# Optimization experiments

Measured on AMD Instinct MI355X. Metric: run time of the kernel, lower is better.

Reference implementation:

```python
import jax, jax.numpy as jnp
import numpy as np

D_MODEL = 128; D_STATE = 64; D_CONV = 4; EXPAND = 2; HEADDIM = 32; NGROUPS = 1
D_INNER = EXPAND * D_MODEL            # 256
NHEADS = D_INNER // HEADDIM           # 8
CONV_DIM = D_INNER + 2 * NGROUPS * D_STATE   # 384 (x, B, C streams)
D_IN_PROJ = 2 * D_INNER + 2 * NGROUPS * D_STATE + NHEADS  # 648 (z, xBC, dt)
EPS = 1e-5


def setup_inputs() -> dict:
    key = jax.random.key(0)
    ks = jax.random.split(key, 8)
    B, L = 8, 4096
    x = jax.random.normal(ks[0], (B, L, D_MODEL), jnp.float32)
    norm_w = jnp.ones((D_MODEL,), jnp.float32)
    in_proj_w = jax.random.normal(ks[1], (D_IN_PROJ, D_MODEL), jnp.float32) * (D_MODEL ** -0.5)
    conv_w = jax.random.normal(ks[2], (CONV_DIM, D_CONV), jnp.float32) * (D_CONV ** -0.5)
    conv_b = jnp.zeros((CONV_DIM,), jnp.float32)
    dt_bias = jax.random.uniform(ks[3], (NHEADS,), jnp.float32, -4.0, -1.0)
    A_log = jnp.log(jax.random.uniform(ks[4], (NHEADS,), jnp.float32, 1.0, 16.0))
    D = jnp.ones((NHEADS,), jnp.float32)
    gnorm_w = jnp.ones((D_INNER,), jnp.float32)
    out_proj_w = jax.random.normal(ks[5], (D_MODEL, D_INNER), jnp.float32) * (D_INNER ** -0.5)
    return dict(x=x, norm_w=norm_w, in_proj_w=in_proj_w, conv_w=conv_w, conv_b=conv_b,
                dt_bias=dt_bias, A_log=A_log, D=D, gnorm_w=gnorm_w, out_proj_w=out_proj_w)


def _rmsnorm(x, w):
    return x * jax.lax.rsqrt(jnp.mean(x * x, axis=-1, keepdims=True) + EPS) * w


def _causal_dw_conv(x, w, b):
    # x: [B,L,C]; w: [C,K]; depthwise causal conv along L
    K = w.shape[1]
    xp = jnp.pad(x, ((0, 0), (K - 1, 0), (0, 0)))
    kern = jnp.transpose(w)[:, None, :]  # [K,1,C] for WIO with groups=C
    out = jax.lax.conv_general_dilated(
        xp, kern, window_strides=(1,), padding='VALID',
        dimension_numbers=('NWC', 'WIO', 'NWC'),
        feature_group_count=w.shape[0])
    return out + b


def _ssm(xh, dt, Bm, Cm, A):
    # xh: [B,L,H,P]; dt: [B,L,H]; Bm, Cm: [B,L,N]; A: [H]
    def step(h, inp):
        x_t, dt_t, B_t, C_t = inp
        dA = jnp.exp(dt_t * A)                                   # [B,H]
        h = h * dA[..., None, None] + (dt_t[..., None] * x_t)[..., None] * B_t[:, None, None, :]
        y = jnp.einsum('bhpn,bn->bhp', h, C_t)
        return h, y
    Bsz, L, H, P = xh.shape
    N = Bm.shape[-1]
    h0 = jnp.zeros((Bsz, H, P, N), xh.dtype)
    xs = (xh.transpose(1, 0, 2, 3), dt.transpose(1, 0, 2),
          Bm.transpose(1, 0, 2), Cm.transpose(1, 0, 2))
    _, ys = jax.lax.scan(step, h0, xs)
    return ys.transpose(1, 0, 2, 3)  # [B,L,H,P]


def reference(x, norm_w, in_proj_w, conv_w, conv_b, dt_bias, A_log, D, gnorm_w, out_proj_w):
    xn = _rmsnorm(x, norm_w)
    zxbcdt = xn @ in_proj_w.T                                    # [B,L,648]
    z, xBC, dt = jnp.split(zxbcdt, [D_INNER, D_INNER + CONV_DIM], axis=-1)
    dt = jax.nn.softplus(dt + dt_bias)                           # [B,L,H]
    xBC = jax.nn.silu(_causal_dw_conv(xBC, conv_w, conv_b))
    xs, Bm, Cm = jnp.split(xBC, [D_INNER, D_INNER + NGROUPS * D_STATE], axis=-1)
    Bsz, L, _ = x.shape
    xh = xs.reshape(Bsz, L, NHEADS, HEADDIM)
    A = -jnp.exp(A_log)                                          # [H]
    y = _ssm(xh, dt, Bm, Cm, A) + D[None, None, :, None] * xh    # D skip per head
    y = y.reshape(Bsz, L, D_INNER)
    y = _rmsnorm(y * jax.nn.silu(z), gnorm_w)                    # gated RMSNorm
    out = y @ out_proj_w.T
    return x + out
```

## Files before the change

### kernel.cpp

```cpp
#include <hip/hip_runtime.h>

#define DM    128
#define DI    256
#define NH    8
#define HD    32
#define NS    64
#define CDIM  384
#define DPROJ 648
#define LSEQ  4096
#define NB    8
#define NTOK  32768
#define LC    64
#define NC    64
#define EPSF  1e-5f
#define LOG2E 1.4426950408889634f

typedef __bf16 bf16;
typedef bf16  bf16x8 __attribute__((ext_vector_type(8)));
typedef bf16  bf16x4 __attribute__((ext_vector_type(4)));
typedef short short8 __attribute__((ext_vector_type(8)));
typedef float f32x4  __attribute__((ext_vector_type(4)));

__device__ __forceinline__ unsigned short f2bfbits(float f) {
    unsigned int u = __float_as_uint(f);
    unsigned int r = u + 0x7FFFu + ((u >> 16) & 1u);
    return (unsigned short)(r >> 16);
}
__device__ __forceinline__ float bfbits2f(unsigned short u) {
    return __uint_as_float(((unsigned int)u) << 16);
}

__global__ __launch_bounds__(256) void k_prep(const float* __restrict__ w1,
                                              const float* __restrict__ w2,
                                              const float* __restrict__ gw,
                                              unsigned short* __restrict__ w1g,
                                              unsigned short* __restrict__ w2f) {
    int i = blockIdx.x * 256 + threadIdx.x;
    if (i < 640 * DM) {
        int f = i >> 9, r = i & 511;
        int lane = r >> 3, jj = r & 7;
        int ns = f >> 2, kk = f & 3;
        int n = ns * 16 + (lane & 15), k = kk * 32 + (lane >> 4) * 8 + jj;
        w1g[i] = f2bfbits(w1[(size_t)n * DM + k]);
    } else {
        int j = i - 640 * DM;
        if (j < DM * DI) {
            int f = j >> 9, r = j & 511;
            int lane = r >> 3, jj = r & 7;
            int kk = f >> 3, nt = f & 7;
            int fr = lane & 15, ko = lane >> 4;
            int n = nt * 16 + fr, k = kk * 32 + ko * 8 + jj;
            w2f[j] = f2bfbits(w2[(size_t)n * DI + k] * gw[k]);
        }
    }
}

__global__ __launch_bounds__(256, 4) void k_gemm1(const float* __restrict__ x,
                                                  const float* __restrict__ nw,
                                                  const float* __restrict__ w1,
                                                  const float* __restrict__ dtb,
                                                  const unsigned short* __restrict__ w1g,
                                                  unsigned short* __restrict__ zb,
                                                  unsigned short* __restrict__ xbc,
                                                  float* __restrict__ dtf) {
    __shared__ float Xs[64][132];
    __shared__ float Wd[8][132];
    const int t = threadIdx.x;
    const int wave = t >> 6, lane = t & 63;
    const int m0 = blockIdx.x * 64;
    {
        int row = t >> 5, col = (t & 31) * 4;
        *(float4*)&Wd[row][col] = *(const float4*)(w1 + (size_t)(640 + row) * DM + col);
    }
    const float nw0 = nw[lane * 2], nw1 = nw[lane * 2 + 1];
    #pragma unroll
    for (int i = 0; i < 16; i++) {
        int r = wave * 16 + i;
        const float* xr = x + (size_t)(m0 + r) * DM + lane * 2;
        float v0 = xr[0], v1 = xr[1];
        float ss = v0 * v0 + v1 * v1;
        #pragma unroll
        for (int o = 32; o; o >>= 1) ss += __shfl_xor(ss, o);
        float rs = rsqrtf(ss * (1.0f / DM) + EPSF);
        Xs[r][lane * 2]     = v0 * rs * nw0;
        Xs[r][lane * 2 + 1] = v1 * rs * nw1;
    }
    __syncthreads();
    {
        const int h = lane >> 3, ks = lane & 7;
        const float dtbh = dtb[h];
        #pragma unroll
        for (int i = 0; i < 16; i++) {
            int r = wave * 16 + i;
            float acc = 0.f;
            #pragma unroll
            for (int q = 0; q < 4; q++) {
                float4 xv = *(const float4*)&Xs[r][ks * 16 + q * 4];
                float4 wv = *(const float4*)&Wd[h][ks * 16 + q * 4];
                acc = fmaf(xv.x, wv.x, acc); acc = fmaf(xv.y, wv.y, acc);
                acc = fmaf(xv.z, wv.z, acc); acc = fmaf(xv.w, wv.w, acc);
            }
            acc += __shfl_xor(acc, 1);
            acc += __shfl_xor(acc, 2);
            acc += __shfl_xor(acc, 4);
            if (ks == 0) {
                float v = acc + dtbh;
                dtf[(size_t)(m0 + r) * NH + h] = (v > 20.f) ? v : log1pf(expf(v));
            }
        }
    }
    const int wm = wave >> 1, wn = wave & 1;
    const int fr = lane & 15, ko = lane >> 4;
    bf16x8 a[2][4];
    #pragma unroll
    for (int mt = 0; mt < 2; mt++)
        #pragma unroll
        for (int kk = 0; kk < 4; kk++) {
            const float* src = &Xs[wm * 32 + mt * 16 + fr][kk * 32 + ko * 8];
            float4 lo = *(const float4*)src, hi = *(const float4*)(src + 4);
            bf16x8 af;
            af[0] = (bf16)lo.x; af[1] = (bf16)lo.y; af[2] = (bf16)lo.z; af[3] = (bf16)lo.w;
            af[4] = (bf16)hi.x; af[5] = (bf16)hi.y; af[6] = (bf16)hi.z; af[7] = (bf16)hi.w;
            a[mt][kk] = af;
        }
    for (int nt = 0; nt < 10; nt++) {
        const unsigned short* wb = w1g + (((size_t)(nt * 4 + wn * 2) * 4) << 9) + lane * 8;
        f32x4 acc[2][2] = {};
        #pragma unroll
        for (int kk = 0; kk < 4; kk++) {
            bf16x8 b0 = *(const bf16x8*)(wb + ((size_t)kk << 9));
            bf16x8 b1 = *(const bf16x8*)(wb + ((size_t)(4 + kk) << 9));
            acc[0][0] = __builtin_amdgcn_mfma_f32_16x16x32_bf16(a[0][kk], b0, acc[0][0], 0, 0, 0);
            acc[1][0] = __builtin_amdgcn_mfma_f32_16x16x32_bf16(a[1][kk], b0, acc[1][0], 0, 0, 0);
            acc[0][1] = __builtin_amdgcn_mfma_f32_16x16x32_bf16(a[0][kk], b1, acc[0][1], 0, 0, 0);
            acc[1][1] = __builtin_amdgcn_mfma_f32_16x16x32_bf16(a[1][kk], b1, acc[1][1], 0, 0, 0);
        }
        unsigned short* dst; int ld, nc0;
        if (nt < 4) { dst = zb;  ld = DI;   nc0 = nt * 64; }
        else        { dst = xbc; ld = CDIM; nc0 = nt * 64 - 256; }
        #pragma unroll
        for (int mt = 0; mt < 2; mt++)
            #pragma unroll
            for (int ntt = 0; ntt < 2; ntt++) {
                int n = nc0 + wn * 32 + ntt * 16 + fr;
                #pragma unroll
                for (int rr = 0; rr < 4; rr++) {
                    int m = m0 + wm * 32 + mt * 16 + ko * 4 + rr;
                    dst[(size_t)m * ld + n] = f2bfbits(acc[mt][ntt][rr]);
                }
            }
    }
}

__global__ __launch_bounds__(384) void k_conv(const unsigned short* __restrict__ xbc,
                                              const float* __restrict__ cw,
                                              const float* __restrict__ cb,
                                              unsigned short* __restrict__ bcA,
                                              unsigned short* __restrict__ xT,
                                              unsigned short* __restrict__ bT) {
    __shared__ __align__(16) unsigned short L[320][72];
    const int c = threadIdx.x;
    const int t0 = blockIdx.x * 64;
    const int l0 = t0 & (LSEQ - 1);
    float4 wv = *(const float4*)(cw + c * 4);
    float bias = cb[c];
    const unsigned short* in = xbc + (size_t)t0 * CDIM + c;
    float h1 = 0.f, h2 = 0.f, h3 = 0.f;
    if (l0) {
        h1 = bfbits2f(in[-CDIM]);
        h2 = bfbits2f(in[-2 * CDIM]);
        h3 = bfbits2f(in[-3 * CDIM]);
    }
    short8 pk;
    #pragma unroll 8
    for (int t = 0; t < 64; t++) {
        float x0 = bfbits2f(in[(size_t)t * CDIM]);
        float acc = bias;
        acc = fmaf(x0, wv.w, acc);
        acc = fmaf(h1, wv.z, acc);
        acc = fmaf(h2, wv.y, acc);
        acc = fmaf(h3, wv.x, acc);
        float s = acc / (1.f + expf(-acc));
        unsigned short us = f2bfbits(s);
        if (c >= 256) bcA[(size_t)(t0 + t) * 128 + (c - 256)] = us;
        pk[t & 7] = (short)us;
        if (c < 320 && (t & 7) == 7) *(short8*)&L[c][t - 7] = pk;
        h3 = h2; h2 = h1; h1 = x0;
    }
    __syncthreads();
    #pragma unroll
    for (int it = 0; it < 7; it++) {
        int idx = it * 384 + c;
        if (idx < 2560) {
            int row = idx >> 3, tc = (idx & 7) * 8;
            short8 v = *(const short8*)&L[row][tc];
            unsigned short* dst = (row < 256)
                ? xT + (size_t)row * NTOK + t0 + tc
                : bT + (size_t)(row - 256) * NTOK + t0 + tc;
            *(short8*)dst = v;
        }
    }
}

__global__ __launch_bounds__(256, 4) void k_ssd1(const unsigned short* __restrict__ bT,
                                                 const unsigned short* __restrict__ xT,
                                                 const float* __restrict__ dtf,
                                                 const float* __restrict__ alog,
                                                 unsigned short* __restrict__ hst,
                                                 float* __restrict__ dAp) {
    __shared__ __align__(16) float wl[4][64];
    const int bh = blockIdx.x >> 4, cg = blockIdx.x & 15;
    const int b = bh >> 3, h = bh & 7;
    const int wave = threadIdx.x >> 6, lane = threadIdx.x & 63;
    const int c = cg * 4 + wave;
    const size_t tok0 = (size_t)b * LSEQ + c * LC;
    const float A = -expf(alog[h]);
    float dt = dtf[(tok0 + lane) * NH + h];
    float q = dt * A * LOG2E;
    #pragma unroll
    for (int o = 1; o <= 32; o <<= 1) {
        float tmp = __shfl_up(q, o);
        if (lane >= o) q += tmp;
    }
    float qL = __shfl(q, 63);
    wl[wave][lane] = exp2f(qL - q) * dt;
    if (lane == 0) dAp[(size_t)bh * NC + c] = exp2f(qL);
    const int m = lane & 15, ko = lane >> 4;
    f32x4 hacc[4][2] = {};
    #pragma unroll
    for (int kh = 0; kh < 2; kh++) {
        bf16x8 xb[2];
        #pragma unroll
        for (int pi = 0; pi < 2; pi++)
            xb[pi] = *(const bf16x8*)(xT + (size_t)(h * HD + pi * 16 + m) * NTOK + tok0 + kh * 32 + ko * 8);
        f32x4 w0 = *(const f32x4*)&wl[wave][kh * 32 + ko * 8];
        f32x4 w1 = *(const f32x4*)&wl[wave][kh * 32 + ko * 8 + 4];
        #pragma unroll
        for (int ni = 0; ni < 4; ni++) {
            bf16x8 bv = *(const bf16x8*)(bT + (size_t)(ni * 16 + m) * NTOK + tok0 + kh * 32 + ko * 8);
            bf16x8 af;
            #pragma unroll
            for (int j = 0; j < 4; j++) af[j] = (bf16)((float)bv[j] * w0[j]);
            #pragma unroll
            for (int j = 0; j < 4; j++) af[4 + j] = (bf16)((float)bv[4 + j] * w1[j]);
            #pragma unroll
            for (int pi = 0; pi < 2; pi++)
                hacc[ni][pi] = __builtin_amdgcn_mfma_f32_16x16x32_bf16(af, xb[pi], hacc[ni][pi], 0, 0, 0);
        }
    }
    unsigned short* hb = hst + (((size_t)bh * NC + c) << 11);
    #pragma unroll
    for (int ni = 0; ni < 4; ni++)
        #pragma unroll
        for (int pi = 0; pi < 2; pi++) {
            bf16x4 pv;
            #pragma unroll
            for (int r = 0; r < 4; r++) pv[r] = (bf16)hacc[ni][pi][r];
            *(bf16x4*)(hb + (pi * 16 + m) * 64 + ni * 16 + ko * 4) = pv;
        }
}

__global__ __launch_bounds__(256) void k_ssm2(unsigned short* __restrict__ hst,
                                              const float* __restrict__ dAp) {
    __shared__ float dl[NC];
    const int bh = blockIdx.x >> 3, seg = blockIdx.x & 7;
    const int s = seg * 256 + threadIdx.x;
    if (threadIdx.x < NC) dl[threadIdx.x] = dAp[(size_t)bh * NC + threadIdx.x];
    __syncthreads();
    unsigned short* p = hst + ((size_t)bh * NC << 11) + s;
    float r = 0.f;
    float v0 = bfbits2f(p[0]);
    float v1 = bfbits2f(p[(size_t)1 << 11]);
    float v2 = bfbits2f(p[(size_t)2 << 11]);
    float v3 = bfbits2f(p[(size_t)3 << 11]);
    for (int c = 0; c < NC; c += 4) {
        float t;
        t = v0; if (c + 4 < NC) v0 = bfbits2f(p[(size_t)(c + 4) << 11]);
        p[(size_t)c << 11] = f2bfbits(r);       r = fmaf(r, dl[c], t);
        t = v1; if (c + 5 < NC) v1 = bfbits2f(p[(size_t)(c + 5) << 11]);
        p[(size_t)(c + 1) << 11] = f2bfbits(r); r = fmaf(r, dl[c + 1], t);
        t = v2; if (c + 6 < NC) v2 = bfbits2f(p[(size_t)(c + 6) << 11]);
        p[(size_t)(c + 2) << 11] = f2bfbits(r); r = fmaf(r, dl[c + 2], t);
        t = v3; if (c + 7 < NC) v3 = bfbits2f(p[(size_t)(c + 7) << 11]);
        p[(size_t)(c + 3) << 11] = f2bfbits(r); r = fmaf(r, dl[c + 3], t);
    }
}

__global__ __launch_bounds__(256, 2) void k_ssd3(const unsigned short* __restrict__ bcA,
                                                 const unsigned short* __restrict__ xT,
                                                 const float* __restrict__ dtf,
                                                 const float* __restrict__ alog,
                                                 const unsigned short* __restrict__ hst,
                                                 const float* __restrict__ Dw,
                                                 unsigned short* __restrict__ ybb) {
    __shared__ __align__(16) bf16 Pl[4][64 * 72];
    __shared__ __align__(16) float ql[4][64];
    __shared__ __align__(16) float dl[4][64];
    const int bh = blockIdx.x >> 4, cg = blockIdx.x & 15;
    const int b = bh >> 3, h = bh & 7;
    const int wave = threadIdx.x >> 6, lane = threadIdx.x & 63;
    const int c = cg * 4 + wave;
    const size_t tok0 = (size_t)b * LSEQ + c * LC;
    const float A = -expf(alog[h]);
    const float Dh = Dw[h];
    float dt = dtf[(tok0 + lane) * NH + h];
    float q = dt * A * LOG2E;
    #pragma unroll
    for (int o = 1; o <= 32; o <<= 1) {
        float tmp = __shfl_up(q, o);
        if (lane >= o) q += tmp;
    }
    ql[wave][lane] = q;
    dl[wave][lane] = dt;
    const int m = lane & 15, ko = lane >> 4;
    bf16x8 cf[4][2];
    #pragma unroll
    for (int ti = 0; ti < 4; ti++)
        #pragma unroll
        for (int kh = 0; kh < 2; kh++)
            cf[ti][kh] = *(const bf16x8*)(bcA + (tok0 + ti * 16 + m) * 128 + 64 + kh * 32 + ko * 8);
    f32x4 gt[4][4] = {};
    #pragma unroll
    for (int kh = 0; kh < 2; kh++) {
        bf16x8 bfg[4];
        #pragma unroll
        for (int si = 0; si < 4; si++)
            bfg[si] = *(const bf16x8*)(bcA + (tok0 + si * 16 + m) * 128 + kh * 32 + ko * 8);
        #pragma unroll
        for (int ti = 0; ti < 4; ti++)
            #pragma unroll
            for (int si = 0; si < 4; si++)
                gt[ti][si] = __builtin_amdgcn_mfma_f32_16x16x32_bf16(bfg[si], cf[ti][kh], gt[ti][si], 0, 0, 0);
    }
    float qt[4];
    #pragma unroll
    for (int ti = 0; ti < 4; ti++) qt[ti] = ql[wave][ti * 16 + m];
    #pragma unroll
    for (int si = 0; si < 4; si++) {
        f32x4 qs = *(const f32x4*)&ql[wave][si * 16 + ko * 4];
        f32x4 ds = *(const f32x4*)&dl[wave][si * 16 + ko * 4];
        #pragma unroll
        for (int ti = 0; ti < 4; ti++) {
            bf16x4 pv = {};
            if (si <= ti) {
                const int t = ti * 16 + m;
                #pragma unroll
                for (int r = 0; r < 4; r++) {
                    int s = si * 16 + ko * 4 + r;
                    float p = 0.f;
                    if (s <= t) {
                        p = exp2f(qt[ti] - qs[r]) * ds[r] * gt[ti][si][r];
                        if (s == t) p += Dh;
                    }
                    pv[r] = (bf16)p;
                }
            }
            *(bf16x4*)&Pl[wave][(ti * 16 + m) * 72 + si * 16 + ko * 4] = pv;
        }
    }
    f32x4 et[4];
    #pragma unroll
    for (int ti = 0; ti < 4; ti++) {
        f32x4 qv = *(const f32x4*)&ql[wave][ti * 16 + ko * 4];
        #pragma unroll
        for (int r = 0; r < 4; r++) et[ti][r] = exp2f(qv[r]);
    }
    const size_t hbase = ((size_t)bh * NC + c) << 11;
    f32x4 ya[4][2] = {}, ua[4][2] = {};
    #pragma unroll
    for (int kh = 0; kh < 2; kh++) {
        bf16x8 xb[2], hb2[2];
        #pragma unroll
        for (int pi = 0; pi < 2; pi++) {
            xb[pi]  = *(const bf16x8*)(xT + (size_t)(h * HD + pi * 16 + m) * NTOK + tok0 + kh * 32 + ko * 8);
            hb2[pi] = *(const bf16x8*)(hst + hbase + (pi * 16 + m) * 64 + kh * 32 + ko * 8);
        }
        #pragma unroll
        for (int ti = 0; ti < 4; ti++) {
            bf16x8 pa = *(const bf16x8*)&Pl[wave][(ti * 16 + m) * 72 + kh * 32 + ko * 8];
            #pragma unroll
            for (int pi = 0; pi < 2; pi++) {
                ya[ti][pi] = __builtin_amdgcn_mfma_f32_16x16x32_bf16(pa, xb[pi], ya[ti][pi], 0, 0, 0);
                ua[ti][pi] = __builtin_amdgcn_mfma_f32_16x16x32_bf16(cf[ti][kh], hb2[pi], ua[ti][pi], 0, 0, 0);
            }
        }
    }
    unsigned short* yrow = ybb + tok0 * DI + h * HD;
    #pragma unroll
    for (int ti = 0; ti < 4; ti++)
        #pragma unroll
        for (int pi = 0; pi < 2; pi++)
            #pragma unroll
            for (int r = 0; r < 4; r++) {
                int t = ti * 16 + ko * 4 + r;
                yrow[(size_t)t * DI + pi * 16 + m] =
                    f2bfbits(ya[ti][pi][r] + et[ti][r] * ua[ti][pi][r]);
            }
}

__global__ __launch_bounds__(256, 4) void k_gemm2g(const unsigned short* __restrict__ ybb,
                                                   const unsigned short* __restrict__ zb,
                                                   const unsigned short* __restrict__ w2f,
                                                   const float* __restrict__ xin,
                                                   float* __restrict__ out) {
    const int t = threadIdx.x;
    const int wave = t >> 6, lane = t & 63;
    const int fr = lane & 15, ko = lane >> 4;
    const int m0 = blockIdx.x * 64 + wave * 16;
    const size_t rowo = (size_t)(m0 + fr) * DI;
    float ss = 0.f;
    bf16x8 gb[8];
    #pragma unroll
    for (int kk = 0; kk < 8; kk++) {
        int co = kk * 32 + ko * 8;
        bf16x8 yv = *(const bf16x8*)(ybb + rowo + co);
        bf16x8 zv = *(const bf16x8*)(zb + rowo + co);
        #pragma unroll
        for (int j = 0; j < 8; j++) {
            float z = (float)zv[j];
            float g = (float)yv[j] * (z / (1.f + expf(-z)));
            ss += g * g;
            gb[kk][j] = (bf16)g;
        }
    }
    ss += __shfl_xor(ss, 16);
    ss += __shfl_xor(ss, 32);
    const float rs = rsqrtf(ss * (1.0f / DI) + EPSF);
    #pragma unroll
    for (int kk = 0; kk < 8; kk++)
        #pragma unroll
        for (int j = 0; j < 8; j++)
            gb[kk][j] = (bf16)((float)gb[kk][j] * rs);
    const unsigned short* wp = w2f + (size_t)lane * 8;
    f32x4 acc[8] = {};
    #pragma unroll
    for (int kk = 0; kk < 8; kk++) {
        #pragma unroll
        for (int nt = 0; nt < 8; nt++) {
            bf16x8 bfr = *(const bf16x8*)(wp + (((size_t)kk * 8 + nt) << 9));
            acc[nt] = __builtin_amdgcn_mfma_f32_16x16x32_bf16(gb[kk], bfr, acc[nt], 0, 0, 0);
        }
    }
    #pragma unroll
    for (int nt = 0; nt < 8; nt++) {
        int n = nt * 16 + fr;
        #pragma unroll
        for (int rr = 0; rr < 4; rr++) {
            int m = m0 + ko * 4 + rr;
            out[(size_t)m * DM + n] = xin[(size_t)m * DM + n] + acc[nt][rr];
        }
    }
}

extern "C" void kernel_launch(void* const* d_in, const int* in_sizes, int n_in,
                              void* d_out, int out_size, void* d_ws, size_t ws_size,
                              hipStream_t stream) {
    const float* x   = (const float*)d_in[0];
    const float* nw  = (const float*)d_in[1];
    const float* w1  = (const float*)d_in[2];
    const float* cw  = (const float*)d_in[3];
    const float* cb  = (const float*)d_in[4];
    const float* dtb = (const float*)d_in[5];
    const float* al  = (const float*)d_in[6];
    const float* Dw  = (const float*)d_in[7];
    const float* gw  = (const float*)d_in[8];
    const float* w2  = (const float*)d_in[9];
    float* out = (float*)d_out;

    float* ws = (float*)d_ws;
    float*  dAp = ws;
    float*  dtf = dAp + NB * NH * NC;
    unsigned short* hst = (unsigned short*)(dtf + (size_t)NTOK * NH);
    unsigned short* zb  = hst + (size_t)NB * NH * NC * 2048;
    unsigned short* xbc = zb + (size_t)NTOK * DI;
    unsigned short* bcA = xbc + (size_t)NTOK * CDIM;
    unsigned short* xT  = bcA + (size_t)NTOK * 128;
    unsigned short* bT  = xT + (size_t)DI * NTOK;
    unsigned short* ybb = bT + (size_t)64 * NTOK;
    unsigned short* w1g = ybb + (size_t)NTOK * DI;
    unsigned short* w2f = w1g + (size_t)640 * DM;

    k_prep<<<(640 * DM + DM * DI + 255) / 256, 256, 0, stream>>>(w1, w2, gw, w1g, w2f);
    k_gemm1<<<NTOK / 64, 256, 0, stream>>>(x, nw, w1, dtb, w1g, zb, xbc, dtf);
    k_conv<<<NTOK / 64, 384, 0, stream>>>(xbc, cw, cb, bcA, xT, bT);
    k_ssd1<<<NB * NH * (NC / 4), 256, 0, stream>>>(bT, xT, dtf, al, hst, dAp);
    k_ssm2<<<NB * NH * 8, 256, 0, stream>>>(hst, dAp);
    k_ssd3<<<NB * NH * (NC / 4), 256, 0, stream>>>(bcA, xT, dtf, al, hst, Dw, ybb);
    k_gemm2g<<<NTOK / 64, 256, 0, stream>>>(ybb, zb, w2f, x, out);
}
```

Measured before the change: 194.2 us.

## Fuse conv and chunk-state SSD kernels; split gemm1 N across two blocks

The depthwise conv kernel now also computes the per-chunk SSD state (formerly k_ssd1). It reads x and B straight from the shared-memory tile it just produced, so the bT buffer and its global round trip are gone and one launch is removed. Separately, gemm1 gets a second grid dimension that splits its 10 N-tiles into two halves, with only the first half doing the dt projection. This doubles block count for more parallelism, at the cost of recomputing the RMSNorm and the X tile loads in both halves.

Result: faster. 189.1 us (-2.7%).

```diff
diff --git a/kernel.cpp b/kernel.cpp
--- a/kernel.cpp
+++ b/kernel.cpp
@@ -68,7 +68,8 @@
     const int t = threadIdx.x;
     const int wave = t >> 6, lane = t & 63;
     const int m0 = blockIdx.x * 64;
-    {
+    const int ny = blockIdx.y;
+    if (ny == 0) {
         int row = t >> 5, col = (t & 31) * 4;
         *(float4*)&Wd[row][col] = *(const float4*)(w1 + (size_t)(640 + row) * DM + col);
     }
@@ -86,7 +87,7 @@
         Xs[r][lane * 2 + 1] = v1 * rs * nw1;
     }
     __syncthreads();
-    {
+    if (ny == 0) {
         const int h = lane >> 3, ks = lane & 7;
         const float dtbh = dtb[h];
         #pragma unroll
@@ -123,7 +124,8 @@
             af[4] = (bf16)hi.x; af[5] = (bf16)hi.y; af[6] = (bf16)hi.z; af[7] = (bf16)hi.w;
             a[mt][kk] = af;
         }
-    for (int nt = 0; nt < 10; nt++) {
+    for (int i = 0; i < 5; i++) {
+        int nt = ny * 5 + i;
         const unsigned short* wb = w1g + (((size_t)(nt * 4 + wn * 2) * 4) << 9) + lane * 8;
         f32x4 acc[2][2] = {};
         #pragma unroll
@@ -152,70 +154,62 @@
     }
 }
 
-__global__ __launch_bounds__(384) void k_conv(const unsigned short* __restrict__ xbc,
-                                              const float* __restrict__ cw,
-                                              const float* __restrict__ cb,
-                                              unsigned short* __restrict__ bcA,
-                                              unsigned short* __restrict__ xT,
-                                              unsigned short* __restrict__ bT) {
+__global__ __launch_bounds__(512) void k_conv1(const unsigned short* __restrict__ xbc,
+                                               const float* __restrict__ cw,
+                                               const float* __restrict__ cb,
+                                               const float* __restrict__ dtf,
+                                               const float* __restrict__ alog,
+                                               unsigned short* __restrict__ bcA,
+                                               unsigned short* __restrict__ xT,
+                                               unsigned short* __restrict__ hst,
+                                               float* __restrict__ dAp) {
     __shared__ __align__(16) unsigned short L[320][72];
-    const int c = threadIdx.x;
+    __shared__ float wlh[NH][64];
+    const int tid = threadIdx.x;
     const int t0 = blockIdx.x * 64;
-    const int l0 = t0 & (LSEQ - 1);
-    float4 wv = *(const float4*)(cw + c * 4);
-    float bias = cb[c];
-    const unsigned short* in = xbc + (size_t)t0 * CDIM + c;
-    float h1 = 0.f, h2 = 0.f, h3 = 0.f;
-    if (l0) {
-        h1 = bfbits2f(in[-CDIM]);
-        h2 = bfbits2f(in[-2 * CDIM]);
-        h3 = bfbits2f(in[-3 * CDIM]);
-    }
-    short8 pk;
-    #pragma unroll 8
-    for (int t = 0; t < 64; t++) {
-        float x0 = bfbits2f(in[(size_t)t * CDIM]);
-        float acc = bias;
-        acc = fmaf(x0, wv.w, acc);
-        acc = fmaf(h1, wv.z, acc);
-        acc = fmaf(h2, wv.y, acc);
-        acc = fmaf(h3, wv.x, acc);
-        float s = acc / (1.f + expf(-acc));
-        unsigned short us = f2bfbits(s);
-        if (c >= 256) bcA[(size_t)(t0 + t) * 128 + (c - 256)] = us;
-        pk[t & 7] = (short)us;
-        if (c < 320 && (t & 7) == 7) *(short8*)&L[c][t - 7] = pk;
-        h3 = h2; h2 = h1; h1 = x0;
+    if (tid < CDIM) {
+        const int ch = tid;
+        const int l0 = t0 & (LSEQ - 1);
+        float4 wv = *(const float4*)(cw + ch * 4);
+        float bias = cb[ch];
+        const unsigned short* in = xbc + (size_t)t0 * CDIM + ch;
+        float h1 = 0.f, h2 = 0.f, h3 = 0.f;
+        if (l0) {
+            h1 = bfbits2f(in[-CDIM]);
+            h2 = bfbits2f(in[-2 * CDIM]);
+            h3 = bfbits2f(in[-3 * CDIM]);
+        }
+        short8 pk;
+        #pragma unroll 8
+        for (int t = 0; t < 64; t++) {
+            float x0 = bfbits2f(in[(size_t)t * CDIM]);
+            float acc = bias;
+            acc = fmaf(x0, wv.w, acc);
+            acc = fmaf(h1, wv.z, acc);
+            acc = fmaf(h2, wv.y, acc);
+            acc = fmaf(h3, wv.x, acc);
+            float s = acc / (1.f + expf(-acc));
+            unsigned short us = f2bfbits(s);
+            if (ch >= 256) bcA[(size_t)(t0 + t) * 128 + (ch - 256)] = us;
+            pk[t & 7] = (short)us;
+            if (ch < 320 && (t & 7) == 7) *(short8*)&L[ch][t - 7] = pk;
+            h3 = h2; h2 = h1; h1 = x0;
+        }
     }
     __syncthreads();
-    #pragma unroll
-    for (int it = 0; it < 7; it++) {
-        int idx = it * 384 + c;
-        if (idx < 2560) {
+    {
+        int idx = tid;
+        #pragma unroll
+        for (int it = 0; it < 4; it++, idx += 512) {
             int row = idx >> 3, tc = (idx & 7) * 8;
-            short8 v = *(const short8*)&L[row][tc];
-            unsigned short* dst = (row < 256)
-                ? xT + (size_t)row * NTOK + t0 + tc
-                : bT + (size_t)(row - 256) * NTOK + t0 + tc;
-            *(short8*)dst = v;
-        }
-    }
-}
-
-__global__ __launch_bounds__(256, 4) void k_ssd1(const unsigned short* __restrict__ bT,
-                                                 const unsigned short* __restrict__ xT,
-                                                 const float* __restrict__ dtf,
-                                                 const float* __restrict__ alog,
-                                                 unsigned short* __restrict__ hst,
-                                                 float* __restrict__ dAp) {
-    __shared__ __align__(16) float wl[4][64];
-    const int bh = blockIdx.x >> 4, cg = blockIdx.x & 15;
-    const int b = bh >> 3, h = bh & 7;
-    const int wave = threadIdx.x >> 6, lane = threadIdx.x & 63;
-    const int c = cg * 4 + wave;
-    const size_t tok0 = (size_t)b * LSEQ + c * LC;
+            *(short8*)(xT + (size_t)row * NTOK + t0 + tc) = *(const short8*)&L[row][tc];
+        }
+    }
+    const int h = tid >> 6, lane = tid & 63;
+    const int b = blockIdx.x >> 6, c = blockIdx.x & 63;
+    const int bh = b * NH + h;
     const float A = -expf(alog[h]);
-    float dt = dtf[(tok0 + lane) * NH + h];
+    float dt = dtf[(size_t)(t0 + lane) * NH + h];
     float q = dt * A * LOG2E;
     #pragma unroll
     for (int o = 1; o <= 32; o <<= 1) {
@@ -223,7 +217,7 @@
         if (lane >= o) q += tmp;
     }
     float qL = __shfl(q, 63);
-    wl[wave][lane] = exp2f(qL - q) * dt;
+    wlh[h][lane] = exp2f(qL - q) * dt;
     if (lane == 0) dAp[(size_t)bh * NC + c] = exp2f(qL);
     const int m = lane & 15, ko = lane >> 4;
     f32x4 hacc[4][2] = {};
@@ -232,17 +226,17 @@
         bf16x8 xb[2];
         #pragma unroll
         for (int pi = 0; pi < 2; pi++)
-            xb[pi] = *(const bf16x8*)(xT + (size_t)(h * HD + pi * 16 + m) * NTOK + tok0 + kh * 32 + ko * 8);
-        f32x4 w0 = *(const f32x4*)&wl[wave][kh * 32 + ko * 8];
-        f32x4 w1 = *(const f32x4*)&wl[wave][kh * 32 + ko * 8 + 4];
+            xb[pi] = *(const bf16x8*)&L[h * HD + pi * 16 + m][kh * 32 + ko * 8];
+        f32x4 w0 = *(const f32x4*)&wlh[h][kh * 32 + ko * 8];
+        f32x4 w1v = *(const f32x4*)&wlh[h][kh * 32 + ko * 8 + 4];
         #pragma unroll
         for (int ni = 0; ni < 4; ni++) {
-            bf16x8 bv = *(const bf16x8*)(bT + (size_t)(ni * 16 + m) * NTOK + tok0 + kh * 32 + ko * 8);
+            bf16x8 bv = *(const bf16x8*)&L[256 + ni * 16 + m][kh * 32 + ko * 8];
             bf16x8 af;
             #pragma unroll
             for (int j = 0; j < 4; j++) af[j] = (bf16)((float)bv[j] * w0[j]);
             #pragma unroll
-            for (int j = 0; j < 4; j++) af[4 + j] = (bf16)((float)bv[4 + j] * w1[j]);
+            for (int j = 0; j < 4; j++) af[4 + j] = (bf16)((float)bv[4 + j] * w1v[j]);
             #pragma unroll
             for (int pi = 0; pi < 2; pi++)
                 hacc[ni][pi] = __builtin_amdgcn_mfma_f32_16x16x32_bf16(af, xb[pi], hacc[ni][pi], 0, 0, 0);
@@ -475,15 +469,13 @@
     unsigned short* xbc = zb + (size_t)NTOK * DI;
     unsigned short* bcA = xbc + (size_t)NTOK * CDIM;
     unsigned short* xT  = bcA + (size_t)NTOK * 128;
-    unsigned short* bT  = xT + (size_t)DI * NTOK;
-    unsigned short* ybb = bT + (size_t)64 * NTOK;
+    unsigned short* ybb = xT + (size_t)DI * NTOK;
     unsigned short* w1g = ybb + (size_t)NTOK * DI;
     unsigned short* w2f = w1g + (size_t)640 * DM;
 
     k_prep<<<(640 * DM + DM * DI + 255) / 256, 256, 0, stream>>>(w1, w2, gw, w1g, w2f);
-    k_gemm1<<<NTOK / 64, 256, 0, stream>>>(x, nw, w1, dtb, w1g, zb, xbc, dtf);
-    k_conv<<<NTOK / 64, 384, 0, stream>>>(xbc, cw, cb, bcA, xT, bT);
-    k_ssd1<<<NB * NH * (NC / 4), 256, 0, stream>>>(bT, xT, dtf, al, hst, dAp);
+    k_gemm1<<<dim3(NTOK / 64, 2), 256, 0, stream>>>(x, nw, w1, dtb, w1g, zb, xbc, dtf);
+    k_conv1<<<NTOK / 64, 512, 0, stream>>>(xbc, cw, cb, dtf, al, bcA, xT, hst, dAp);
     k_ssm2<<<NB * NH * 8, 256, 0, stream>>>(hst, dAp);
     k_ssd3<<<NB * NH * (NC / 4), 256, 0, stream>>>(bcA, xT, dtf, al, hst, Dw, ybb);
     k_gemm2g<<<NTOK / 64, 256, 0, stream>>>(ybb, zb, w2f, x, out);
```
